# Performance work log

Hardware: AMD Instinct MI355X
Metric: run time of the kernel (lower is better)

## Reference

```python
import jax, jax.numpy as jnp
import numpy as np

K_MASK = -2.3819763e+38
NUM_KV_HEADS = 4
SOFT_CAP = 50.0
WINDOW = 1024
ROPE_BASE = 10000.0
ROPE_SCALE = 1.0


def rms_norm(x, scale=None, eps=1e-6):
    var = jnp.mean(jnp.square(x), axis=-1, keepdims=True)
    normed = x * jax.lax.rsqrt(var + eps)
    if scale is not None:
        normed = normed * (1.0 + scale)
    return normed


def apply_rope(x, positions):
    # x: [B, T, N, H], positions: [B, T]
    head_dim = x.shape[-1]
    fraction = 2.0 * jnp.arange(head_dim // 2, dtype=jnp.float32) / head_dim
    timescale = ROPE_BASE ** fraction  # [H/2]
    sinusoid = positions[..., None, None].astype(jnp.float32) / timescale / ROPE_SCALE  # [B,T,1,H/2]
    sin, cos = jnp.sin(sinusoid), jnp.cos(sinusoid)
    first, second = jnp.split(x, 2, axis=-1)
    return jnp.concatenate([first * cos - second * sin,
                            second * cos + first * sin], axis=-1).astype(x.dtype)


def setup_inputs() -> dict:
    key = jax.random.key(0)
    ks = jax.random.split(key, 8)
    B, T, D, N, K, H, F = 2, 2048, 2048, 8, NUM_KV_HEADS, 256, 8192
    CACHE = 4096
    x = jax.random.normal(ks[0], (B, T, D), dtype=jnp.float32)
    segment_pos = jnp.broadcast_to(jnp.arange(T, dtype=jnp.int32)[None, :], (B, T))
    # causal mask over cache slots: after scatter, slot s (< T) holds position s; slots >= T are empty
    s_idx = jnp.arange(CACHE)
    t_idx = jnp.arange(T)
    attn_mask = (s_idx[None, :] <= t_idx[:, None]) & (s_idx[None, :] < T)
    attn_mask = jnp.broadcast_to(attn_mask[None], (B, T, CACHE))
    cache_k = jnp.zeros((B, CACHE, K, H), dtype=jnp.float32)
    cache_v = jnp.zeros((B, CACHE, K, H), dtype=jnp.float32)
    cache_positions = jnp.zeros((B, CACHE), dtype=jnp.int32)
    end_index = jnp.zeros((B,), dtype=jnp.int32)
    w_q = jax.random.normal(ks[1], (N, D, H), dtype=jnp.float32) * 0.02
    w_kv = jax.random.normal(ks[2], (2, K, D, H), dtype=jnp.float32) * 0.02
    w_attn_vec = jax.random.normal(ks[3], (N, H, D), dtype=jnp.float32) * 0.02
    w_gating = jax.random.normal(ks[4], (2, F, D), dtype=jnp.float32) * 0.02
    w_linear = jax.random.normal(ks[5], (F, D), dtype=jnp.float32) * 0.02
    return {
        'x': x, 'segment_pos': segment_pos, 'attn_mask': attn_mask,
        'cache_k': cache_k, 'cache_v': cache_v,
        'cache_positions': cache_positions, 'end_index': end_index,
        'w_q': w_q, 'w_kv': w_kv, 'w_attn_vec': w_attn_vec,
        'q_norm_scale': jnp.zeros((H,), dtype=jnp.float32),
        'k_norm_scale': jnp.zeros((H,), dtype=jnp.float32),
        'pre_attn_scale': jnp.zeros((D,), dtype=jnp.float32),
        'post_attn_scale': jnp.zeros((D,), dtype=jnp.float32),
        'pre_ffw_scale': jnp.zeros((D,), dtype=jnp.float32),
        'post_ffw_scale': jnp.zeros((D,), dtype=jnp.float32),
        'w_gating': w_gating, 'w_linear': w_linear,
        'skip_scale': jnp.ones((1,), dtype=jnp.float32),
    }


def reference(x, segment_pos, attn_mask, cache_k, cache_v, cache_positions, end_index,
              w_q, w_kv, w_attn_vec, q_norm_scale, k_norm_scale,
              pre_attn_scale, post_attn_scale, pre_ffw_scale, post_ffw_scale,
              w_gating, w_linear, skip_scale):
    B, T, D = x.shape
    cache_size = cache_v.shape[1]

    h = rms_norm(x, pre_attn_scale)

    # --- attention ---
    q = jnp.einsum('BTD,NDH->BTNH', h, w_q)
    q = rms_norm(q, q_norm_scale)
    q = apply_rope(q, segment_pos)

    k, v = jnp.einsum('BSD,CKDH->CBSKH', h, w_kv)
    k = rms_norm(k, k_norm_scale)
    v = rms_norm(v, None)
    k = apply_rope(k, segment_pos)

    # KV-cache scatter (ring-buffer indexing)
    idx = (end_index[:, None] + jnp.arange(T)[None, :]) % cache_size  # [B,T]
    bidx = jnp.arange(B)[:, None]
    v = cache_v.at[bidx, idx].set(v)              # [B,S,K,H]
    k = cache_k.at[bidx, idx].set(k)
    cache_pos = cache_positions.at[bidx, idx].set(segment_pos)  # [B,S]

    # GQA logits
    N, H = q.shape[2], q.shape[3]
    G = N // NUM_KV_HEADS
    qg = q.reshape(B, T, NUM_KV_HEADS, G, H)
    logits = jnp.einsum('BTKGH,BSKH->BTKGS', qg, k).reshape(B, T, N, cache_size)

    # soft cap
    logits = jnp.tanh(logits / SOFT_CAP) * SOFT_CAP

    # sliding-window mask against cache positions
    sliding = (cache_pos[:, None, :] > segment_pos[:, :, None] - WINDOW) & \
              (cache_pos[:, None, :] < segment_pos[:, :, None] + WINDOW)  # [B,T,S]
    mask = attn_mask & sliding

    padded = jnp.where(mask[:, :, None, :], logits, K_MASK)
    probs = jax.nn.softmax(padded, axis=-1).astype(k.dtype)

    pg = probs.reshape(B, T, NUM_KV_HEADS, G, cache_size)
    encoded = jnp.einsum('BTKGS,BSKH->BTKGH', pg, v).reshape(B, T, N, H)
    attn_out = jnp.einsum('BTNH,NHD->BTD', encoded, w_attn_vec)

    # post-attn norm + residual (skip_scale on the skip connection)
    attn_out = rms_norm(attn_out, post_attn_scale)
    attn_out = x * skip_scale + attn_out

    # --- feed-forward ---
    ffw_in = rms_norm(attn_out, pre_ffw_scale)
    gate = jnp.einsum('BTF,CHF->BTCH', ffw_in, w_gating)  # C=2
    act = jax.nn.gelu(gate[..., 0, :]) * gate[..., 1, :]
    ffw_out = jnp.einsum('BTH,HF->BTF', act, w_linear)
    ffw_out = rms_norm(ffw_out, post_ffw_scale)

    return attn_out + ffw_out
```

## Files before the change

### kernel.cpp

```cpp
#include <hip/hip_runtime.h>


typedef _Float16 h8 __attribute__((ext_vector_type(8)));
typedef _Float16 h4 __attribute__((ext_vector_type(4)));
typedef float f4 __attribute__((ext_vector_type(4)));

#define BDIM 2
#define TDIM 2048
#define DDIM 2048
#define NQ 8
#define NKV 4
#define HDIM 256
#define FDIM 8192
#define MROWS (BDIM * TDIM)
#define WINDOW 1024
#define QS 4096

__device__ inline float gelu_tanh(float x) {
  return 0.5f * x * (1.f + tanhf(0.7978845608028654f * (x + 0.044715f * x * x * x)));
}

__device__ __forceinline__ void g2l16(const _Float16* g, _Float16* l) {
  __builtin_amdgcn_global_load_lds(
      (const __attribute__((address_space(1))) void*)g,
      (__attribute__((address_space(3))) void*)l, 16, 0, 0);
}

__device__ inline float block_sum(float v, float* sbuf) {
#pragma unroll
  for (int off = 32; off; off >>= 1) v += __shfl_xor(v, off, 64);
  __syncthreads();
  if ((threadIdx.x & 63) == 0) sbuf[threadIdx.x >> 6] = v;
  __syncthreads();
  return sbuf[0] + sbuf[1] + sbuf[2] + sbuf[3];
}

template <int EPI>
__global__ __launch_bounds__(256, 4) void gemm_bt(
    const _Float16* __restrict__ A, const _Float16* __restrict__ Bt,
    void* __restrict__ Cout, const _Float16* __restrict__ aux,
    int M, int Nc, int K) {
  __shared__ _Float16 As[128 * 32];
  __shared__ _Float16 Bs[128 * 32];
  const int tid = threadIdx.x;
  const int m0 = blockIdx.y * 128, n0 = blockIdx.x * 128;
  const int w = tid >> 6, lane = tid & 63;
  const int l16 = lane & 15, quad = lane >> 4;
  const int wm = (w >> 1) * 64, wn = (w & 1) * 64;

  f4 acc[4][4];
#pragma unroll
  for (int i = 0; i < 4; i++)
#pragma unroll
    for (int j = 0; j < 4; j++) {
      acc[i][j][0] = 0.f; acc[i][j][1] = 0.f; acc[i][j][2] = 0.f; acc[i][j][3] = 0.f;
    }

  const int lrow = lane >> 2, lcol = (lane & 3) * 8;
  const _Float16* Ag = A + (size_t)(m0 + w * 32 + lrow) * K + lcol;
  const _Float16* Bg = Bt + (size_t)(n0 + w * 32 + lrow) * K + lcol;
  _Float16* AsW = &As[(w * 32) * 32];
  _Float16* BsW = &Bs[(w * 32) * 32];

  for (int k0 = 0; k0 < K; k0 += 32) {
    __syncthreads();
    g2l16(Ag + k0,                  AsW);
    g2l16(Ag + (size_t)16 * K + k0, AsW + 16 * 32);
    g2l16(Bg + k0,                  BsW);
    g2l16(Bg + (size_t)16 * K + k0, BsW + 16 * 32);
    __syncthreads();
    h8 af[4], bf[4];
#pragma unroll
    for (int i = 0; i < 4; i++) af[i] = *(const h8*)&As[(wm + i * 16 + l16) * 32 + quad * 8];
#pragma unroll
    for (int i = 0; i < 4; i++) bf[i] = *(const h8*)&Bs[(wn + i * 16 + l16) * 32 + quad * 8];
#pragma unroll
    for (int mi = 0; mi < 4; mi++)
#pragma unroll
      for (int ni = 0; ni < 4; ni++)
        acc[mi][ni] = __builtin_amdgcn_mfma_f32_16x16x32_f16(af[mi], bf[ni], acc[mi][ni], 0, 0, 0);
  }

#pragma unroll
  for (int mi = 0; mi < 4; mi++)
#pragma unroll
    for (int ni = 0; ni < 4; ni++)
#pragma unroll
      for (int r = 0; r < 4; r++) {
        const int rg = m0 + wm + mi * 16 + quad * 4 + r;
        const int cg = n0 + wn + ni * 16 + l16;
        const size_t idx = (size_t)rg * Nc + cg;
        float v = acc[mi][ni][r];
        if (EPI == 0) {
          ((float*)Cout)[idx] = v;
        } else if (EPI == 1) {
          ((_Float16*)Cout)[idx] = (_Float16)v;
        } else {
          float g = (float)aux[idx];
          ((_Float16*)Cout)[idx] = (_Float16)(gelu_tanh(g) * v);
        }
      }
}

__global__ __launch_bounds__(256) void transpose_cast_kernel(
    const float* __restrict__ in, _Float16* __restrict__ out,
    int R, int C, size_t in_zstride, size_t out_zstride) {
  __shared__ float tile[64][65];
  const float* ip = in + blockIdx.z * in_zstride;
  _Float16* op = out + blockIdx.z * out_zstride;
  const int cb = blockIdx.x * 64, rb = blockIdx.y * 64;
  const int tx = threadIdx.x & 15, ty = threadIdx.x >> 4;
#pragma unroll
  for (int i = 0; i < 4; i++) {
    f4 v = *(const f4*)&ip[(size_t)(rb + ty + 16 * i) * C + cb + tx * 4];
    tile[ty + 16 * i][tx * 4 + 0] = v[0];
    tile[ty + 16 * i][tx * 4 + 1] = v[1];
    tile[ty + 16 * i][tx * 4 + 2] = v[2];
    tile[ty + 16 * i][tx * 4 + 3] = v[3];
  }
  __syncthreads();
#pragma unroll
  for (int i = 0; i < 4; i++) {
    const int c = ty + 16 * i;
    h4 o;
#pragma unroll
    for (int j = 0; j < 4; j++) o[j] = (_Float16)tile[tx * 4 + j][c];
    *(h4*)&op[(size_t)(cb + c) * R + rb + tx * 4] = o;
  }
}

__global__ void cast_fp16_kernel(const float* __restrict__ in,
                                 _Float16* __restrict__ out, int n4) {
  int i = blockIdx.x * 256 + threadIdx.x;
  if (i < n4) {
    f4 v = ((const f4*)in)[i];
    h4 o;
    o[0] = (_Float16)v[0]; o[1] = (_Float16)v[1];
    o[2] = (_Float16)v[2]; o[3] = (_Float16)v[3];
    ((h4*)out)[i] = o;
  }
}

__global__ __launch_bounds__(256) void rmsnorm_fp16_kernel(
    const float* __restrict__ in, const float* __restrict__ scale,
    _Float16* __restrict__ out) {
  __shared__ float sbuf[4];
  const int row = blockIdx.x, tid = threadIdx.x;
  const float* r = in + (size_t)row * 2048;
  f4 a = ((const f4*)r)[tid];
  f4 b = ((const f4*)r)[tid + 256];
  float ss = a[0]*a[0] + a[1]*a[1] + a[2]*a[2] + a[3]*a[3] +
             b[0]*b[0] + b[1]*b[1] + b[2]*b[2] + b[3]*b[3];
  float tot = block_sum(ss, sbuf);
  float rs = rsqrtf(tot * (1.f / 2048.f) + 1e-6f);
  f4 s0 = ((const f4*)scale)[tid];
  f4 s1 = ((const f4*)scale)[tid + 256];
  h4 o0, o1;
#pragma unroll
  for (int j = 0; j < 4; j++) {
    o0[j] = (_Float16)(a[j] * rs * (1.f + s0[j]));
    o1[j] = (_Float16)(b[j] * rs * (1.f + s1[j]));
  }
  ((h4*)(out + (size_t)row * 2048))[tid] = o0;
  ((h4*)(out + (size_t)row * 2048))[tid + 256] = o1;
}

__global__ __launch_bounds__(256) void headnorm_qkv_kernel(
    const float* __restrict__ qkv, _Float16* __restrict__ out,
    const float* __restrict__ qsc, const float* __restrict__ ksc,
    const int* __restrict__ pos_arr) {
  const int inst = blockIdx.x * 4 + (threadIdx.x >> 6);
  const int lane = threadIdx.x & 63;
  const int row = inst >> 4, slot = inst & 15;
  const float* r = qkv + (size_t)row * QS + slot * 256;
  f4 v = ((const f4*)r)[lane];
  float ss = v[0]*v[0] + v[1]*v[1] + v[2]*v[2] + v[3]*v[3];
#pragma unroll
  for (int off = 32; off; off >>= 1) ss += __shfl_xor(ss, off, 64);
  const float rs = rsqrtf(ss * (1.f / 256.f) + 1e-6f);
  const float* scale = (slot < 8) ? qsc : (slot < 12 ? ksc : nullptr);
  f4 nv;
  if (scale) {
    f4 sc = ((const f4*)scale)[lane];
#pragma unroll
    for (int j = 0; j < 4; j++) nv[j] = v[j] * rs * (1.f + sc[j]);
  } else {
#pragma unroll
    for (int j = 0; j < 4; j++) nv[j] = v[j] * rs;
  }
  h4 res;
  if (slot < 12) {
    const float pos = (float)pos_arr[row];
    const bool lo = lane < 32;
#pragma unroll
    for (int j = 0; j < 4; j++) {
      float partner = __shfl_xor(nv[j], 32, 64);
      const int ph = (lane * 4 + j) & 127;
      float it = exp2f((float)ph * -0.103810253f);
      float ang = pos * it;
      float sn, cs;
      sincosf(ang, &sn, &cs);
      res[j] = (_Float16)(lo ? (nv[j] * cs - partner * sn)
                             : (nv[j] * cs + partner * sn));
    }
  } else {
#pragma unroll
    for (int j = 0; j < 4; j++) res[j] = (_Float16)nv[j];
  }
  ((h4*)(out + (size_t)row * QS + slot * 256))[lane] = res;
}

__global__ __launch_bounds__(256) void transpose_v_kernel(
    const _Float16* __restrict__ qkvh, _Float16* __restrict__ vT) {
  __shared__ _Float16 tile[32][33];
  const int z = blockIdx.z;
  const int b = z >> 2, kvh = z & 3;
  const int tb = blockIdx.x * 32, hb = blockIdx.y * 32;
  const int x = threadIdx.x, y = threadIdx.y;
#pragma unroll
  for (int i = 0; i < 4; i++)
    tile[y + 8 * i][x] =
        qkvh[(size_t)(b * TDIM + tb + y + 8 * i) * QS + 3072 + kvh * 256 + hb + x];
  __syncthreads();
#pragma unroll
  for (int i = 0; i < 4; i++)
    vT[((size_t)z * HDIM + hb + y + 8 * i) * TDIM + tb + x] = tile[x][y + 8 * i];
}

__global__ __launch_bounds__(256) void attn_kernel(
    const _Float16* __restrict__ qkvh, const _Float16* __restrict__ vT,
    _Float16* __restrict__ enc) {
  __shared__ _Float16 Ks[32 * 256];
  __shared__ _Float16 Vs[256 * 32];
  __shared__ _Float16 Ps[4][16 * 32];
  const int t0 = blockIdx.x * 64;
  const int n = blockIdx.y;
  const int b = blockIdx.z;
  const int kvh = n >> 1;
  const int tid = threadIdx.x;
  const int w = tid >> 6, lane = tid & 63, l16 = lane & 15, quad = lane >> 4;

  h8 qfrag[8];
  {
    const int trow = t0 + w * 16 + l16;
    const _Float16* qp =
        qkvh + (size_t)(b * TDIM + trow) * QS + n * HDIM + quad * 8;
#pragma unroll
    for (int ks = 0; ks < 8; ks++) qfrag[ks] = *(const h8*)(qp + ks * 32);
  }

  f4 O[16];
#pragma unroll
  for (int i = 0; i < 16; i++) { O[i][0] = 0.f; O[i][1] = 0.f; O[i][2] = 0.f; O[i][3] = 0.f; }
  float m_i[4], l_i[4];
#pragma unroll
  for (int r = 0; r < 4; r++) { m_i[r] = -1e30f; l_i[r] = 0.f; }

  int s_begin = t0 - (WINDOW - 1);
  if (s_begin < 0) s_begin = 0;
  s_begin &= ~31;
  const int s_end = t0 + 64;
  const _Float16* kbase = qkvh + (size_t)b * TDIM * QS + 2048 + kvh * HDIM;
  const _Float16* vbase = vT + ((size_t)(b * NKV + kvh) * HDIM) * TDIM;

  for (int s0 = s_begin; s0 < s_end; s0 += 32) {
    __syncthreads();
#pragma unroll
    for (int p = 0; p < 4; p++) {
      int g = p * 256 + tid;
      {
        int si = g >> 5, hg = (g & 31) << 3;
        *(h8*)&Ks[si * 256 + hg] = *(const h8*)(kbase + (size_t)(s0 + si) * QS + hg);
      }
      {
        int h = g >> 2, sg = (g & 3) << 3;
        *(h8*)&Vs[h * 32 + sg] = *(const h8*)(vbase + (size_t)h * TDIM + s0 + sg);
      }
    }
    __syncthreads();

    float P[2][4], cmax[4];
#pragma unroll
    for (int r = 0; r < 4; r++) cmax[r] = -1e30f;
#pragma unroll
    for (int sc = 0; sc < 2; sc++) {
      f4 lg; lg[0] = 0.f; lg[1] = 0.f; lg[2] = 0.f; lg[3] = 0.f;
#pragma unroll
      for (int ks = 0; ks < 8; ks++) {
        h8 kb = *(const h8*)&Ks[(sc * 16 + l16) * 256 + ks * 32 + quad * 8];
        lg = __builtin_amdgcn_mfma_f32_16x16x32_f16(qfrag[ks], kb, lg, 0, 0, 0);
      }
      const int scol = s0 + sc * 16 + l16;
#pragma unroll
      for (int r = 0; r < 4; r++) {
        const int trow = t0 + w * 16 + quad * 4 + r;
        float xv = 50.f * tanhf(lg[r] * 0.02f);
        bool valid = (scol <= trow) && (scol > trow - WINDOW);
        P[sc][r] = valid ? xv : -1e30f;
        cmax[r] = fmaxf(cmax[r], P[sc][r]);
      }
    }
#pragma unroll
    for (int off = 1; off < 16; off <<= 1)
#pragma unroll
      for (int r = 0; r < 4; r++) cmax[r] = fmaxf(cmax[r], __shfl_xor(cmax[r], off, 16));
    float alpha[4], psum[4];
#pragma unroll
    for (int r = 0; r < 4; r++) {
      float mnew = fmaxf(m_i[r], cmax[r]);
      alpha[r] = __expf(m_i[r] - mnew);
      m_i[r] = mnew;
      psum[r] = 0.f;
    }
#pragma unroll
    for (int sc = 0; sc < 2; sc++)
#pragma unroll
      for (int r = 0; r < 4; r++) {
        float pv = __expf(P[sc][r] - m_i[r]);
        P[sc][r] = pv;
        psum[r] += pv;
      }
#pragma unroll
    for (int off = 1; off < 16; off <<= 1)
#pragma unroll
      for (int r = 0; r < 4; r++) psum[r] += __shfl_xor(psum[r], off, 16);
#pragma unroll
    for (int r = 0; r < 4; r++) l_i[r] = l_i[r] * alpha[r] + psum[r];
#pragma unroll
    for (int i = 0; i < 16; i++)
#pragma unroll
      for (int r = 0; r < 4; r++) O[i][r] *= alpha[r];
#pragma unroll
    for (int sc = 0; sc < 2; sc++)
#pragma unroll
      for (int r = 0; r < 4; r++)
        Ps[w][(quad * 4 + r) * 32 + sc * 16 + l16] = (_Float16)P[sc][r];
    h8 pa = *(const h8*)&Ps[w][l16 * 32 + quad * 8];
#pragma unroll
    for (int ht = 0; ht < 16; ht++) {
      h8 vb = *(const h8*)&Vs[(ht * 16 + l16) * 32 + quad * 8];
      O[ht] = __builtin_amdgcn_mfma_f32_16x16x32_f16(pa, vb, O[ht], 0, 0, 0);
    }
  }

  float invl[4];
#pragma unroll
  for (int r = 0; r < 4; r++) invl[r] = 1.f / l_i[r];
#pragma unroll
  for (int ht = 0; ht < 16; ht++)
#pragma unroll
    for (int r = 0; r < 4; r++) {
      const int trow = t0 + w * 16 + quad * 4 + r;
      enc[((size_t)(b * TDIM + trow)) * (NQ * HDIM) + n * HDIM + ht * 16 + l16] =
          (_Float16)(O[ht][r] * invl[r]);
    }
}

__global__ __launch_bounds__(256) void postattn_kernel(
    const float* __restrict__ attnraw, const float* __restrict__ x,
    const float* __restrict__ post_scale, const float* __restrict__ pre_ffw_scale,
    const float* __restrict__ skip, float* __restrict__ attn_out,
    _Float16* __restrict__ ffw_in) {
  __shared__ float sbuf[4];
  const int row = blockIdx.x, tid = threadIdx.x;
  const float* ar = attnraw + (size_t)row * 2048;
  const float* xr = x + (size_t)row * 2048;
  f4 a0 = ((const f4*)ar)[tid], a1 = ((const f4*)ar)[tid + 256];
  float ss = a0[0]*a0[0] + a0[1]*a0[1] + a0[2]*a0[2] + a0[3]*a0[3] +
             a1[0]*a1[0] + a1[1]*a1[1] + a1[2]*a1[2] + a1[3]*a1[3];
  float tot = block_sum(ss, sbuf);
  float rs = rsqrtf(tot * (1.f / 2048.f) + 1e-6f);
  const float sk = skip[0];
  f4 x0 = ((const f4*)xr)[tid], x1 = ((const f4*)xr)[tid + 256];
  f4 p0 = ((const f4*)post_scale)[tid], p1 = ((const f4*)post_scale)[tid + 256];
  f4 at0, at1;
#pragma unroll
  for (int j = 0; j < 4; j++) {
    at0[j] = x0[j] * sk + a0[j] * rs * (1.f + p0[j]);
    at1[j] = x1[j] * sk + a1[j] * rs * (1.f + p1[j]);
  }
  ((f4*)(attn_out + (size_t)row * 2048))[tid] = at0;
  ((f4*)(attn_out + (size_t)row * 2048))[tid + 256] = at1;
  float ss2 = at0[0]*at0[0] + at0[1]*at0[1] + at0[2]*at0[2] + at0[3]*at0[3] +
              at1[0]*at1[0] + at1[1]*at1[1] + at1[2]*at1[2] + at1[3]*at1[3];
  float tot2 = block_sum(ss2, sbuf);
  float rs2 = rsqrtf(tot2 * (1.f / 2048.f) + 1e-6f);
  f4 f0 = ((const f4*)pre_ffw_scale)[tid], f1 = ((const f4*)pre_ffw_scale)[tid + 256];
  h4 o0, o1;
#pragma unroll
  for (int j = 0; j < 4; j++) {
    o0[j] = (_Float16)(at0[j] * rs2 * (1.f + f0[j]));
    o1[j] = (_Float16)(at1[j] * rs2 * (1.f + f1[j]));
  }
  ((h4*)(ffw_in + (size_t)row * 2048))[tid] = o0;
  ((h4*)(ffw_in + (size_t)row * 2048))[tid + 256] = o1;
}

__global__ __launch_bounds__(256) void final_kernel(
    const float* __restrict__ ffw, const float* __restrict__ attn_out,
    const float* __restrict__ post_ffw_scale, float* __restrict__ out) {
  __shared__ float sbuf[4];
  const int row = blockIdx.x, tid = threadIdx.x;
  const float* fr = ffw + (size_t)row * 2048;
  const float* ar = attn_out + (size_t)row * 2048;
  f4 a0 = ((const f4*)fr)[tid], a1 = ((const f4*)fr)[tid + 256];
  float ss = a0[0]*a0[0] + a0[1]*a0[1] + a0[2]*a0[2] + a0[3]*a0[3] +
             a1[0]*a1[0] + a1[1]*a1[1] + a1[2]*a1[2] + a1[3]*a1[3];
  float tot = block_sum(ss, sbuf);
  float rs = rsqrtf(tot * (1.f / 2048.f) + 1e-6f);
  f4 s0 = ((const f4*)post_ffw_scale)[tid], s1 = ((const f4*)post_ffw_scale)[tid + 256];
  f4 x0 = ((const f4*)ar)[tid], x1 = ((const f4*)ar)[tid + 256];
  f4 o0, o1;
#pragma unroll
  for (int j = 0; j < 4; j++) {
    o0[j] = x0[j] + a0[j] * rs * (1.f + s0[j]);
    o1[j] = x1[j] + a1[j] * rs * (1.f + s1[j]);
  }
  ((f4*)(out + (size_t)row * 2048))[tid] = o0;
  ((f4*)(out + (size_t)row * 2048))[tid + 256] = o1;
}

extern "C" void kernel_launch(void* const* d_in, const int* in_sizes, int n_in,
                              void* d_out, int out_size, void* d_ws, size_t ws_size,
                              hipStream_t stream) {
  (void)in_sizes; (void)n_in; (void)out_size; (void)ws_size;
  const float* x              = (const float*)d_in[0];
  const int*   segment_pos    = (const int*)d_in[1];
  const float* w_q            = (const float*)d_in[7];
  const float* w_kv           = (const float*)d_in[8];
  const float* w_attn_vec     = (const float*)d_in[9];
  const float* q_norm_scale   = (const float*)d_in[10];
  const float* k_norm_scale   = (const float*)d_in[11];
  const float* pre_attn_scale = (const float*)d_in[12];
  const float* post_attn_scale= (const float*)d_in[13];
  const float* pre_ffw_scale  = (const float*)d_in[14];
  const float* post_ffw_scale = (const float*)d_in[15];
  const float* w_gating       = (const float*)d_in[16];
  const float* w_linear       = (const float*)d_in[17];
  const float* skip_scale     = (const float*)d_in[18];

  char* ws = (char*)d_ws;
  const size_t MB = 1024 * 1024;
  _Float16* Wqkv = (_Float16*)(ws + 0);
  _Float16* Wo   = (_Float16*)(ws + 0);
  _Float16* Wg   = (_Float16*)(ws + 0);
  _Float16* Wl   = (_Float16*)(ws + 0);
  _Float16* Hbf  = (_Float16*)(ws + 64 * MB);
  float* attnF   = (float*)(ws + 80 * MB);
  float* qkvf32  = (float*)(ws + 112 * MB);
  _Float16* qkvh = (_Float16*)(ws + 176 * MB);
  _Float16* enc  = (_Float16*)(ws + 208 * MB);
  float* attnraw = (float*)(ws + 224 * MB);
  _Float16* vT   = (_Float16*)(ws + 240 * MB);
  _Float16* gate0= (_Float16*)(ws + 112 * MB);
  _Float16* act  = (_Float16*)(ws + 176 * MB);
  float* ffw     = (float*)(ws + 240 * MB);
  float* outp    = (float*)d_out;

  transpose_cast_kernel<<<dim3(HDIM / 64, DDIM / 64, NQ), 256, 0, stream>>>(
      w_q, Wqkv, DDIM, HDIM, (size_t)DDIM * HDIM, (size_t)HDIM * DDIM);
  transpose_cast_kernel<<<dim3(HDIM / 64, DDIM / 64, NKV), 256, 0, stream>>>(
      w_kv, Wqkv + (size_t)2048 * DDIM, DDIM, HDIM,
      (size_t)DDIM * HDIM, (size_t)HDIM * DDIM);
  transpose_cast_kernel<<<dim3(HDIM / 64, DDIM / 64, NKV), 256, 0, stream>>>(
      w_kv + (size_t)NKV * DDIM * HDIM, Wqkv + (size_t)3072 * DDIM, DDIM, HDIM,
      (size_t)DDIM * HDIM, (size_t)HDIM * DDIM);
  rmsnorm_fp16_kernel<<<MROWS, 256, 0, stream>>>(x, pre_attn_scale, Hbf);
  gemm_bt<0><<<dim3(QS / 128, MROWS / 128), 256, 0, stream>>>(
      Hbf, Wqkv, qkvf32, nullptr, MROWS, QS, DDIM);
  headnorm_qkv_kernel<<<(MROWS * 16) / 4, 256, 0, stream>>>(
      qkvf32, qkvh, q_norm_scale, k_norm_scale, segment_pos);
  transpose_v_kernel<<<dim3(TDIM / 32, HDIM / 32, BDIM * NKV), dim3(32, 8), 0, stream>>>(
      qkvh, vT);
  attn_kernel<<<dim3(TDIM / 64, NQ, BDIM), 256, 0, stream>>>(qkvh, vT, enc);
  transpose_cast_kernel<<<dim3(DDIM / 64, (NQ * HDIM) / 64, 1), 256, 0, stream>>>(
      w_attn_vec, Wo, NQ * HDIM, DDIM, 0, 0);
  gemm_bt<0><<<dim3(DDIM / 128, MROWS / 128), 256, 0, stream>>>(
      enc, Wo, attnraw, nullptr, MROWS, DDIM, NQ * HDIM);
  postattn_kernel<<<MROWS, 256, 0, stream>>>(attnraw, x, post_attn_scale,
                                             pre_ffw_scale, skip_scale, attnF, Hbf);
  cast_fp16_kernel<<<(2 * FDIM * DDIM / 4 + 255) / 256, 256, 0, stream>>>(
      w_gating, Wg, 2 * FDIM * DDIM / 4);
  gemm_bt<1><<<dim3(FDIM / 128, MROWS / 128), 256, 0, stream>>>(
      Hbf, Wg, gate0, nullptr, MROWS, FDIM, DDIM);
  gemm_bt<2><<<dim3(FDIM / 128, MROWS / 128), 256, 0, stream>>>(
      Hbf, Wg + (size_t)FDIM * DDIM, act, gate0, MROWS, FDIM, DDIM);
  transpose_cast_kernel<<<dim3(DDIM / 64, FDIM / 64, 1), 256, 0, stream>>>(
      w_linear, Wl, FDIM, DDIM, 0, 0);
  gemm_bt<0><<<dim3(DDIM / 128, MROWS / 128), 256, 0, stream>>>(
      act, Wl, ffw, nullptr, MROWS, DDIM, FDIM);
  final_kernel<<<MROWS, 256, 0, stream>>>(ffw, attnF, post_ffw_scale, outp);
}
```

Before: 1.272 ms.

## Fuse gate GEMMs with GELU, deepen GEMM K-step, use fp16 intermediates and fast tanh

The two gating GEMMs become one kernel that loads the A tile once, keeps two accumulator sets and applies GELU times the linear branch in the epilogue. This removes the fp16 gate round-trip through memory and the second read of the activations. The generic GEMM now stages 64 of K per sync instead of 32, halving barrier count but using more LDS and a lower occupancy hint. The QKV and final FFW GEMM outputs are written as fp16 instead of fp32 to cut memory traffic, at some cost in precision. Both tanh calls (GELU and the attention soft cap) are rewritten as exp plus reciprocal forms.

```diff
diff --git a/kernel.cpp b/kernel.cpp
--- a/kernel.cpp
+++ b/kernel.cpp
@@ -16,8 +16,10 @@
 #define WINDOW 1024
 #define QS 4096
 
-__device__ inline float gelu_tanh(float x) {
-  return 0.5f * x * (1.f + tanhf(0.7978845608028654f * (x + 0.044715f * x * x * x)));
+__device__ __forceinline__ float gelu_fast(float x) {
+  float u = 1.5957691216057308f * (x + 0.044715f * x * x * x);
+  float e = __expf(u);
+  return x * e / (e + 1.f);
 }
 
 __device__ __forceinline__ void g2l16(const _Float16* g, _Float16* l) {
@@ -36,12 +38,11 @@
 }
 
 template <int EPI>
-__global__ __launch_bounds__(256, 4) void gemm_bt(
+__global__ __launch_bounds__(256, 3) void gemm_bt(
     const _Float16* __restrict__ A, const _Float16* __restrict__ Bt,
-    void* __restrict__ Cout, const _Float16* __restrict__ aux,
-    int M, int Nc, int K) {
-  __shared__ _Float16 As[128 * 32];
-  __shared__ _Float16 Bs[128 * 32];
+    void* __restrict__ Cout, int M, int Nc, int K) {
+  __shared__ _Float16 As[2 * 128 * 32];
+  __shared__ _Float16 Bs[2 * 128 * 32];
   const int tid = threadIdx.x;
   const int m0 = blockIdx.y * 128, n0 = blockIdx.x * 128;
   const int w = tid >> 6, lane = tid & 63;
@@ -59,26 +60,34 @@
   const int lrow = lane >> 2, lcol = (lane & 3) * 8;
   const _Float16* Ag = A + (size_t)(m0 + w * 32 + lrow) * K + lcol;
   const _Float16* Bg = Bt + (size_t)(n0 + w * 32 + lrow) * K + lcol;
-  _Float16* AsW = &As[(w * 32) * 32];
-  _Float16* BsW = &Bs[(w * 32) * 32];
-
-  for (int k0 = 0; k0 < K; k0 += 32) {
+  _Float16* AsW = &As[w * 32 * 32];
+  _Float16* BsW = &Bs[w * 32 * 32];
+
+  for (int k0 = 0; k0 < K; k0 += 64) {
     __syncthreads();
-    g2l16(Ag + k0,                  AsW);
-    g2l16(Ag + (size_t)16 * K + k0, AsW + 16 * 32);
-    g2l16(Bg + k0,                  BsW);
-    g2l16(Bg + (size_t)16 * K + k0, BsW + 16 * 32);
+#pragma unroll
+    for (int s = 0; s < 2; s++) {
+      g2l16(Ag + k0 + s * 32,                  AsW + s * 4096);
+      g2l16(Ag + (size_t)16 * K + k0 + s * 32, AsW + s * 4096 + 16 * 32);
+      g2l16(Bg + k0 + s * 32,                  BsW + s * 4096);
+      g2l16(Bg + (size_t)16 * K + k0 + s * 32, BsW + s * 4096 + 16 * 32);
+    }
     __syncthreads();
-    h8 af[4], bf[4];
-#pragma unroll
-    for (int i = 0; i < 4; i++) af[i] = *(const h8*)&As[(wm + i * 16 + l16) * 32 + quad * 8];
-#pragma unroll
-    for (int i = 0; i < 4; i++) bf[i] = *(const h8*)&Bs[(wn + i * 16 + l16) * 32 + quad * 8];
-#pragma unroll
-    for (int mi = 0; mi < 4; mi++)
-#pragma unroll
-      for (int ni = 0; ni < 4; ni++)
-        acc[mi][ni] = __builtin_amdgcn_mfma_f32_16x16x32_f16(af[mi], bf[ni], acc[mi][ni], 0, 0, 0);
+#pragma unroll
+    for (int s = 0; s < 2; s++) {
+      h8 af[4], bf[4];
+#pragma unroll
+      for (int i = 0; i < 4; i++)
+        af[i] = *(const h8*)&As[s * 4096 + (wm + i * 16 + l16) * 32 + quad * 8];
+#pragma unroll
+      for (int i = 0; i < 4; i++)
+        bf[i] = *(const h8*)&Bs[s * 4096 + (wn + i * 16 + l16) * 32 + quad * 8];
+#pragma unroll
+      for (int mi = 0; mi < 4; mi++)
+#pragma unroll
+        for (int ni = 0; ni < 4; ni++)
+          acc[mi][ni] = __builtin_amdgcn_mfma_f32_16x16x32_f16(af[mi], bf[ni], acc[mi][ni], 0, 0, 0);
+    }
   }
 
 #pragma unroll
@@ -90,15 +99,84 @@
         const int rg = m0 + wm + mi * 16 + quad * 4 + r;
         const int cg = n0 + wn + ni * 16 + l16;
         const size_t idx = (size_t)rg * Nc + cg;
-        float v = acc[mi][ni][r];
-        if (EPI == 0) {
-          ((float*)Cout)[idx] = v;
-        } else if (EPI == 1) {
-          ((_Float16*)Cout)[idx] = (_Float16)v;
-        } else {
-          float g = (float)aux[idx];
-          ((_Float16*)Cout)[idx] = (_Float16)(gelu_tanh(g) * v);
+        if (EPI == 0) ((float*)Cout)[idx] = acc[mi][ni][r];
+        else          ((_Float16*)Cout)[idx] = (_Float16)acc[mi][ni][r];
+      }
+}
+
+__global__ __launch_bounds__(256, 2) void gemm_gate(
+    const _Float16* __restrict__ A, const _Float16* __restrict__ B0,
+    const _Float16* __restrict__ B1, _Float16* __restrict__ act,
+    int M, int Nc, int K) {
+  __shared__ _Float16 As[2 * 128 * 32];
+  __shared__ _Float16 Bs0[2 * 128 * 32];
+  __shared__ _Float16 Bs1[2 * 128 * 32];
+  const int tid = threadIdx.x;
+  const int m0 = blockIdx.y * 128, n0 = blockIdx.x * 128;
+  const int w = tid >> 6, lane = tid & 63;
+  const int l16 = lane & 15, quad = lane >> 4;
+  const int wm = (w >> 1) * 64, wn = (w & 1) * 64;
+
+  f4 acc0[4][4], acc1[4][4];
+#pragma unroll
+  for (int i = 0; i < 4; i++)
+#pragma unroll
+    for (int j = 0; j < 4; j++) {
+      acc0[i][j][0] = 0.f; acc0[i][j][1] = 0.f; acc0[i][j][2] = 0.f; acc0[i][j][3] = 0.f;
+      acc1[i][j][0] = 0.f; acc1[i][j][1] = 0.f; acc1[i][j][2] = 0.f; acc1[i][j][3] = 0.f;
+    }
+
+  const int lrow = lane >> 2, lcol = (lane & 3) * 8;
+  const _Float16* Ag  = A  + (size_t)(m0 + w * 32 + lrow) * K + lcol;
+  const _Float16* B0g = B0 + (size_t)(n0 + w * 32 + lrow) * K + lcol;
+  const _Float16* B1g = B1 + (size_t)(n0 + w * 32 + lrow) * K + lcol;
+  _Float16* AsW  = &As[w * 32 * 32];
+  _Float16* Bs0W = &Bs0[w * 32 * 32];
+  _Float16* Bs1W = &Bs1[w * 32 * 32];
+
+  for (int k0 = 0; k0 < K; k0 += 64) {
+    __syncthreads();
+#pragma unroll
+    for (int s = 0; s < 2; s++) {
+      g2l16(Ag + k0 + s * 32,                   AsW + s * 4096);
+      g2l16(Ag + (size_t)16 * K + k0 + s * 32,  AsW + s * 4096 + 16 * 32);
+      g2l16(B0g + k0 + s * 32,                  Bs0W + s * 4096);
+      g2l16(B0g + (size_t)16 * K + k0 + s * 32, Bs0W + s * 4096 + 16 * 32);
+      g2l16(B1g + k0 + s * 32,                  Bs1W + s * 4096);
+      g2l16(B1g + (size_t)16 * K + k0 + s * 32, Bs1W + s * 4096 + 16 * 32);
+    }
+    __syncthreads();
+#pragma unroll
+    for (int s = 0; s < 2; s++) {
+      h8 af[4], b0f[4], b1f[4];
+#pragma unroll
+      for (int i = 0; i < 4; i++)
+        af[i] = *(const h8*)&As[s * 4096 + (wm + i * 16 + l16) * 32 + quad * 8];
+#pragma unroll
+      for (int i = 0; i < 4; i++) {
+        b0f[i] = *(const h8*)&Bs0[s * 4096 + (wn + i * 16 + l16) * 32 + quad * 8];
+        b1f[i] = *(const h8*)&Bs1[s * 4096 + (wn + i * 16 + l16) * 32 + quad * 8];
+      }
+#pragma unroll
+      for (int mi = 0; mi < 4; mi++)
+#pragma unroll
+        for (int ni = 0; ni < 4; ni++) {
+          acc0[mi][ni] = __builtin_amdgcn_mfma_f32_16x16x32_f16(af[mi], b0f[ni], acc0[mi][ni], 0, 0, 0);
+          acc1[mi][ni] = __builtin_amdgcn_mfma_f32_16x16x32_f16(af[mi], b1f[ni], acc1[mi][ni], 0, 0, 0);
         }
+    }
+  }
+
+#pragma unroll
+  for (int mi = 0; mi < 4; mi++)
+#pragma unroll
+    for (int ni = 0; ni < 4; ni++)
+#pragma unroll
+      for (int r = 0; r < 4; r++) {
+        const int rg = m0 + wm + mi * 16 + quad * 4 + r;
+        const int cg = n0 + wn + ni * 16 + l16;
+        act[(size_t)rg * Nc + cg] =
+            (_Float16)(gelu_fast(acc0[mi][ni][r]) * acc1[mi][ni][r]);
       }
 }
 
@@ -166,14 +244,17 @@
 }
 
 __global__ __launch_bounds__(256) void headnorm_qkv_kernel(
-    const float* __restrict__ qkv, _Float16* __restrict__ out,
+    const _Float16* __restrict__ qkv, _Float16* __restrict__ out,
     const float* __restrict__ qsc, const float* __restrict__ ksc,
     const int* __restrict__ pos_arr) {
   const int inst = blockIdx.x * 4 + (threadIdx.x >> 6);
   const int lane = threadIdx.x & 63;
   const int row = inst >> 4, slot = inst & 15;
-  const float* r = qkv + (size_t)row * QS + slot * 256;
-  f4 v = ((const f4*)r)[lane];
+  const _Float16* r = qkv + (size_t)row * QS + slot * 256;
+  h4 vh = ((const h4*)r)[lane];
+  f4 v;
+#pragma unroll
+  for (int j = 0; j < 4; j++) v[j] = (float)vh[j];
   float ss = v[0]*v[0] + v[1]*v[1] + v[2]*v[2] + v[3]*v[3];
 #pragma unroll
   for (int off = 32; off; off >>= 1) ss += __shfl_xor(ss, off, 64);
@@ -294,7 +375,8 @@
 #pragma unroll
       for (int r = 0; r < 4; r++) {
         const int trow = t0 + w * 16 + quad * 4 + r;
-        float xv = 50.f * tanhf(lg[r] * 0.02f);
+        float t = __expf(lg[r] * 0.04f);
+        float xv = 50.f - 100.f * __builtin_amdgcn_rcpf(t + 1.f);
         bool valid = (scol <= trow) && (scol > trow - WINDOW);
         P[sc][r] = valid ? xv : -1e30f;
         cmax[r] = fmaxf(cmax[r], P[sc][r]);
@@ -397,13 +479,16 @@
 }
 
 __global__ __launch_bounds__(256) void final_kernel(
-    const float* __restrict__ ffw, const float* __restrict__ attn_out,
+    const _Float16* __restrict__ ffw, const float* __restrict__ attn_out,
     const float* __restrict__ post_ffw_scale, float* __restrict__ out) {
   __shared__ float sbuf[4];
   const int row = blockIdx.x, tid = threadIdx.x;
-  const float* fr = ffw + (size_t)row * 2048;
+  const _Float16* fr = ffw + (size_t)row * 2048;
   const float* ar = attn_out + (size_t)row * 2048;
-  f4 a0 = ((const f4*)fr)[tid], a1 = ((const f4*)fr)[tid + 256];
+  h4 fh0 = ((const h4*)fr)[tid], fh1 = ((const h4*)fr)[tid + 256];
+  f4 a0, a1;
+#pragma unroll
+  for (int j = 0; j < 4; j++) { a0[j] = (float)fh0[j]; a1[j] = (float)fh1[j]; }
   float ss = a0[0]*a0[0] + a0[1]*a0[1] + a0[2]*a0[2] + a0[3]*a0[3] +
              a1[0]*a1[0] + a1[1]*a1[1] + a1[2]*a1[2] + a1[3]*a1[3];
   float tot = block_sum(ss, sbuf);
@@ -441,21 +526,20 @@
 
   char* ws = (char*)d_ws;
   const size_t MB = 1024 * 1024;
-  _Float16* Wqkv = (_Float16*)(ws + 0);
-  _Float16* Wo   = (_Float16*)(ws + 0);
-  _Float16* Wg   = (_Float16*)(ws + 0);
-  _Float16* Wl   = (_Float16*)(ws + 0);
-  _Float16* Hbf  = (_Float16*)(ws + 64 * MB);
-  float* attnF   = (float*)(ws + 80 * MB);
-  float* qkvf32  = (float*)(ws + 112 * MB);
-  _Float16* qkvh = (_Float16*)(ws + 176 * MB);
-  _Float16* enc  = (_Float16*)(ws + 208 * MB);
-  float* attnraw = (float*)(ws + 224 * MB);
-  _Float16* vT   = (_Float16*)(ws + 240 * MB);
-  _Float16* gate0= (_Float16*)(ws + 112 * MB);
-  _Float16* act  = (_Float16*)(ws + 176 * MB);
-  float* ffw     = (float*)(ws + 240 * MB);
-  float* outp    = (float*)d_out;
+  _Float16* Wqkv  = (_Float16*)(ws + 0);
+  _Float16* Wo    = (_Float16*)(ws + 0);
+  _Float16* Wg    = (_Float16*)(ws + 0);
+  _Float16* Wl    = (_Float16*)(ws + 0);
+  _Float16* Hbf   = (_Float16*)(ws + 64 * MB);
+  float* attnF    = (float*)(ws + 80 * MB);
+  _Float16* qkvraw= (_Float16*)(ws + 112 * MB);
+  _Float16* qkvh  = (_Float16*)(ws + 144 * MB);
+  _Float16* enc   = (_Float16*)(ws + 176 * MB);
+  float* attnraw  = (float*)(ws + 192 * MB);
+  _Float16* vT    = (_Float16*)(ws + 224 * MB);
+  _Float16* act   = (_Float16*)(ws + 112 * MB);
+  _Float16* ffw   = (_Float16*)(ws + 192 * MB);
+  float* outp     = (float*)d_out;
 
   transpose_cast_kernel<<<dim3(HDIM / 64, DDIM / 64, NQ), 256, 0, stream>>>(
       w_q, Wqkv, DDIM, HDIM, (size_t)DDIM * HDIM, (size_t)HDIM * DDIM);
@@ -466,28 +550,26 @@
       w_kv + (size_t)NKV * DDIM * HDIM, Wqkv + (size_t)3072 * DDIM, DDIM, HDIM,
       (size_t)DDIM * HDIM, (size_t)HDIM * DDIM);
   rmsnorm_fp16_kernel<<<MROWS, 256, 0, stream>>>(x, pre_attn_scale, Hbf);
-  gemm_bt<0><<<dim3(QS / 128, MROWS / 128), 256, 0, stream>>>(
-      Hbf, Wqkv, qkvf32, nullptr, MROWS, QS, DDIM);
+  gemm_bt<1><<<dim3(QS / 128, MROWS / 128), 256, 0, stream>>>(
+      Hbf, Wqkv, qkvraw, MROWS, QS, DDIM);
   headnorm_qkv_kernel<<<(MROWS * 16) / 4, 256, 0, stream>>>(
-      qkvf32, qkvh, q_norm_scale, k_norm_scale, segment_pos);
+      qkvraw, qkvh, q_norm_scale, k_norm_scale, segment_pos);
   transpose_v_kernel<<<dim3(TDIM / 32, HDIM / 32, BDIM * NKV), dim3(32, 8), 0, stream>>>(
       qkvh, vT);
   attn_kernel<<<dim3(TDIM / 64, NQ, BDIM), 256, 0, stream>>>(qkvh, vT, enc);
   transpose_cast_kernel<<<dim3(DDIM / 64, (NQ * HDIM) / 64, 1), 256, 0, stream>>>(
       w_attn_vec, Wo, NQ * HDIM, DDIM, 0, 0);
   gemm_bt<0><<<dim3(DDIM / 128, MROWS / 128), 256, 0, stream>>>(
-      enc, Wo, attnraw, nullptr, MROWS, DDIM, NQ * HDIM);
+      enc, Wo, attnraw, MROWS, DDIM, NQ * HDIM);
   postattn_kernel<<<MROWS, 256, 0, stream>>>(attnraw, x, post_attn_scale,
                                              pre_ffw_scale, skip_scale, attnF, Hbf);
   cast_fp16_kernel<<<(2 * FDIM * DDIM / 4 + 255) / 256, 256, 0, stream>>>(
       w_gating, Wg, 2 * FDIM * DDIM / 4);
-  gemm_bt<1><<<dim3(FDIM / 128, MROWS / 128), 256, 0, stream>>>(
-      Hbf, Wg, gate0, nullptr, MROWS, FDIM, DDIM);
-  gemm_bt<2><<<dim3(FDIM / 128, MROWS / 128), 256, 0, stream>>>(
-      Hbf, Wg + (size_t)FDIM * DDIM, act, gate0, MROWS, FDIM, DDIM);
+  gemm_gate<<<dim3(FDIM / 128, MROWS / 128), 256, 0, stream>>>(
+      Hbf, Wg, Wg + (size_t)FDIM * DDIM, act, MROWS, FDIM, DDIM);
   transpose_cast_kernel<<<dim3(DDIM / 64, FDIM / 64, 1), 256, 0, stream>>>(
       w_linear, Wl, FDIM, DDIM, 0, 0);
-  gemm_bt<0><<<dim3(DDIM / 128, MROWS / 128), 256, 0, stream>>>(
-      act, Wl, ffw, nullptr, MROWS, DDIM, FDIM);
+  gemm_bt<1><<<dim3(DDIM / 128, MROWS / 128), 256, 0, stream>>>(
+      act, Wl, ffw, MROWS, DDIM, FDIM);
   final_kernel<<<MROWS, 256, 0, stream>>>(ffw, attnF, post_ffw_scale, outp);
 }
```

Result: faster. 1.131 ms (-11.1%).
